# Performance work log

Hardware: AMD Instinct MI355X
Metric: run time of the kernel (lower is better)

The kernel has to match this reference:

```python
import jax, jax.numpy as jnp
import numpy as np

EPS = 1e-6


def _hungarian(cost):
    """Min-cost rectangular assignment (Kuhn-Munkres with potentials).
    Returns (row_ind, col_ind) matching min(n, m) pairs, like scipy's
    linear_sum_assignment. Cost matrices here are tiny (<= 7x7)."""
    cost = np.asarray(cost, dtype=np.float64)
    transposed = False
    if cost.shape[0] > cost.shape[1]:
        cost = cost.T
        transposed = True
    n, m = cost.shape
    INF = 1e18
    u = np.zeros(n + 1)
    v = np.zeros(m + 1)
    p = np.zeros(m + 1, dtype=np.int64)   # p[j] = row matched to col j (1-indexed)
    way = np.zeros(m + 1, dtype=np.int64)
    for i in range(1, n + 1):
        p[0] = i
        j0 = 0
        minv = np.full(m + 1, INF)
        used = np.zeros(m + 1, dtype=bool)
        while True:
            used[j0] = True
            i0 = p[j0]
            delta = INF
            j1 = 0
            for j in range(1, m + 1):
                if not used[j]:
                    cur = cost[i0 - 1, j - 1] - u[i0] - v[j]
                    if cur < minv[j]:
                        minv[j] = cur
                        way[j] = j0
                    if minv[j] < delta:
                        delta = minv[j]
                        j1 = j
            for j in range(m + 1):
                if used[j]:
                    u[p[j]] += delta
                    v[j] -= delta
                else:
                    minv[j] -= delta
            j0 = j1
            if p[j0] == 0:
                break
        while j0:
            j1 = way[j0]
            p[j0] = p[j1]
            j0 = j1
    rows, cols = [], []
    for j in range(1, m + 1):
        if p[j] != 0:
            rows.append(p[j] - 1)
            cols.append(j - 1)
    if transposed:
        rows, cols = cols, rows
    order = np.argsort(rows)
    return [rows[k] for k in order], [cols[k] for k in order]


def setup_inputs() -> dict:
    key = jax.random.key(0)
    kp, kg, kn = jax.random.split(key, 3)
    B, S, H, W = 32, 8, 256, 256
    pred_attn = jax.random.uniform(kp, (B, S, H, W), dtype=jnp.float32)  # soft slot attention
    gt_masks = jnp.round(jax.random.uniform(kg, (B, S, H, W), dtype=jnp.float32))  # binary GT
    num_objects = jax.random.randint(kn, (B,), 0, 8, dtype=jnp.int32)
    return {"pred_attn": pred_attn, "gt_masks": gt_masks, "num_objects": num_objects}


def _match(dice_mat, num_objects, num_gt):
    """Host-side Hungarian matching on the (negated) dice similarity matrix."""
    cost = -np.asarray(dice_mat)  # (B, P, G)
    nobj = np.asarray(num_objects)
    bi, pi, gi = [], [], []
    for b in range(cost.shape[0]):
        n = int(min(int(nobj[b]), num_gt))
        if n == 0:
            continue
        r, c = _hungarian(cost[b, :, :n])
        bi += [b] * len(r)
        pi += list(r)
        gi += list(c)
    return np.array(bi, np.int64), np.array(pi, np.int64), np.array(gi, np.int64)


def _losses(pred_attn, gt_masks, bi, pi, gi):
    B, S, H, W = pred_attn.shape
    # background dice loss (slot 0)
    bg_p = pred_attn[:, 0].reshape(B, -1)
    bg_g = gt_masks[:, 0].reshape(B, -1)
    inter = (bg_p * bg_g).sum(-1)
    union = bg_p.sum(-1) + bg_g.sum(-1)
    bg_loss = (1.0 - (2.0 * inter + EPS) / (union + EPS)).mean()
    # pairwise dice over all (pred_slot, gt_slot) fg pairs in one einsum
    fg_p = pred_attn[:, 1:].reshape(B, S - 1, -1)  # (B, P, HW)
    fg_g = gt_masks[:, 1:].reshape(B, S - 1, -1)   # (B, G, HW)
    inter_m = jnp.einsum('bpn,bgn->bpg', fg_p, fg_g)
    union_m = fg_p.sum(-1)[:, :, None] + fg_g.sum(-1)[:, None, :]
    dice_m = (2.0 * inter_m + EPS) / (union_m + EPS)  # (B, P, G)
    if bi.size:
        fg_loss = (1.0 - dice_m[bi, pi, gi]).mean()
    else:
        fg_loss = jnp.float32(0.0)
    return bg_loss, fg_loss, dice_m


def reference(pred_attn, gt_masks, num_objects):
    BG_WEIGHT, FG_WEIGHT = 1.0, 1.0
    B, S, H, W = pred_attn.shape
    # build dice similarity matrix once (vectorized; replaces the double loop)
    _, _, dice_m = _losses(pred_attn, gt_masks,
                           np.array([], np.int64), np.array([], np.int64), np.array([], np.int64))
    bi, pi, gi = _match(jax.lax.stop_gradient(dice_m), num_objects, S - 1)
    bg_loss, fg_loss, _ = _losses(pred_attn, gt_masks, bi, pi, gi)
    return BG_WEIGHT * bg_loss + FG_WEIGHT * fg_loss
```

## Files before the change

### kernel.cpp

```cpp
#include <hip/hip_runtime.h>
#include <stdint.h>

#define EPSF 1e-6f

__device__ __forceinline__ float wave_sum_to_lane63(float x) {
  x += __int_as_float(__builtin_amdgcn_update_dpp(0, __float_as_int(x), 0x111, 0xf, 0xf, true));
  x += __int_as_float(__builtin_amdgcn_update_dpp(0, __float_as_int(x), 0x112, 0xf, 0xf, true));
  x += __int_as_float(__builtin_amdgcn_update_dpp(0, __float_as_int(x), 0x114, 0xf, 0xf, true));
  x += __int_as_float(__builtin_amdgcn_update_dpp(0, __float_as_int(x), 0x118, 0xf, 0xf, true));
  x += __int_as_float(__builtin_amdgcn_update_dpp(0, __float_as_int(x), 0x142, 0xa, 0xf, false));
  x += __int_as_float(__builtin_amdgcn_update_dpp(0, __float_as_int(x), 0x143, 0xc, 0xf, false));
  return x;
}

__device__ __forceinline__ float sum4(float4 a) {
  return (a.x + a.y) + (a.z + a.w);
}
__device__ __forceinline__ float dot4(float4 a, float4 b) {
  return a.x * b.x + a.y * b.y + a.z * b.z + a.w * b.w;
}

#define RSZ 1024

__global__ __launch_bounds__(256) void msl_pack(const float* __restrict__ gt,
                                                uint32_t* __restrict__ bits,
                                                int nwords) {
  const int w = blockIdx.x * 256 + threadIdx.x;
  if (w >= nwords) return;
  const float4* src = (const float4*)(gt + (size_t)w * 32);
  uint32_t u = 0;
#pragma unroll
  for (int q = 0; q < 8; ++q) {
    float4 x = src[q];
    u |= (x.x > 0.5f ? 1u : 0u) << (q * 4 + 0);
    u |= (x.y > 0.5f ? 1u : 0u) << (q * 4 + 1);
    u |= (x.z > 0.5f ? 1u : 0u) << (q * 4 + 2);
    u |= (x.w > 0.5f ? 1u : 0u) << (q * 4 + 3);
  }
  bits[w] = u;
}

__global__ __launch_bounds__(256) void msl_accum(const float* __restrict__ pred,
                                                 const uint32_t* __restrict__ bits,
                                                 float* __restrict__ acc, int HW) {
  __shared__ float sm[8 * RSZ];
  const int bx   = blockIdx.x;
  const int b    = blockIdx.y;
  const int tid  = threadIdx.x;
  const int wave = tid >> 6;
  const int lane = tid & 63;

  const size_t base = (size_t)b * 8 * (size_t)HW;
  const float* Pr = pred + base + (size_t)bx * RSZ;
  const int wordsPerStream = HW >> 5;
  const int wbase = bx * (RSZ >> 5);

#pragma unroll
  for (int j = 0; j < 2; ++j) {
    const int s = wave * 2 + j;
    const float* sbase = Pr + (size_t)s * HW;
#pragma unroll
    for (int k = 0; k < 4; ++k) {
      const float* gp = sbase + k * 256 + lane * 4;
      float* lp = &sm[s * RSZ + k * 256];
      __builtin_amdgcn_global_load_lds(
          (const __attribute__((address_space(1))) void*)gp,
          (__attribute__((address_space(3))) void*)lp, 16, 0, 0);
    }
  }
  __builtin_amdgcn_s_waitcnt(0x0F70);
  __syncthreads();

  const int t4 = tid * 4;
  float4 pa[8];
#pragma unroll
  for (int p = 0; p < 8; ++p) pa[p] = *(const float4*)&sm[p * RSZ + t4];

  float sp[8], sg[8];
#pragma unroll
  for (int p = 0; p < 8; ++p) sp[p] = sum4(pa[p]);

  float a_bg = 0.0f;
  float af[7][7];
#pragma unroll
  for (int p = 0; p < 7; ++p)
#pragma unroll
    for (int g = 0; g < 7; ++g) af[p][g] = 0.0f;

#pragma unroll
  for (int g = 0; g < 8; ++g) {
    const uint32_t w = bits[(size_t)(b * 8 + g) * wordsPerStream + wbase + (tid >> 3)];
    const uint32_t nib = (w >> ((tid & 7) * 4)) & 0xFu;
    sg[g] = (float)__popc(nib);
    float4 m;
    m.x = (nib & 1u) ? 1.0f : 0.0f;
    m.y = (nib & 2u) ? 1.0f : 0.0f;
    m.z = (nib & 4u) ? 1.0f : 0.0f;
    m.w = (nib & 8u) ? 1.0f : 0.0f;
    if (g == 0) {
      a_bg = dot4(pa[0], m);
    } else {
#pragma unroll
      for (int p = 1; p < 8; ++p)
        af[p - 1][g - 1] += dot4(pa[p], m);
    }
  }

  float v[66];
  v[0] = a_bg;
#pragma unroll
  for (int p = 0; p < 7; ++p)
#pragma unroll
    for (int g = 0; g < 7; ++g) v[1 + p * 7 + g] = af[p][g];
#pragma unroll
  for (int s = 0; s < 8; ++s) { v[50 + s] = sp[s]; v[58 + s] = sg[s]; }

  __syncthreads();
  float* red = sm;
#pragma unroll
  for (int k = 0; k < 66; ++k) {
    float x = wave_sum_to_lane63(v[k]);
    if (lane == 63) red[wave * 66 + k] = x;
  }
  __syncthreads();

  if (tid < 66) {
    float s = red[0 * 66 + tid] + red[1 * 66 + tid] +
              red[2 * 66 + tid] + red[3 * 66 + tid];
    atomicAdd(&acc[b * 66 + tid], s);
  }
}

__global__ __launch_bounds__(1024) void msl_final(const float* __restrict__ acc,
                                                  const int* __restrict__ nobj,
                                                  float* __restrict__ out, int B) {
  __shared__ float a[32][68];
  __shared__ float dp[32][130];
  __shared__ float dice[32][52];
  __shared__ float r_bg[32];
  __shared__ float r_ds[32];
  __shared__ int   r_n[32];

  const int batch = threadIdx.x >> 5;
  const int lane  = threadIdx.x & 31;
  const bool act  = (batch < B);

  if (act) {
    for (int k = lane; k < 66; k += 32) a[batch][k] = acc[batch * 66 + k];
  }
  __syncthreads();

  if (act) {
    for (int k = lane; k < 49; k += 32) {
      int p = k / 7, g = k % 7;
      dice[batch][k] = (2.0f * a[batch][1 + k] + EPSF) /
                       (a[batch][51 + p] + a[batch][59 + g] + EPSF);
    }
    if (lane == 0) {
      float u = a[batch][50] + a[batch][58];
      r_bg[batch] = 1.0f - (2.0f * a[batch][0] + EPSF) / (u + EPSF);
      int n = nobj[batch];
      n = n < 0 ? 0 : (n > 7 ? 7 : n);
      r_n[batch] = n;
      r_ds[batch] = 0.0f;
      dp[batch][0] = 0.0f;
    }
  }
  __syncthreads();
  const int n = act ? r_n[batch] : 0;

  for (int c = 1; c <= 7; ++c) {
    if (act && c <= n) {
      for (int mask = lane; mask < 128; mask += 32) {
        if (__popc(mask) == c) {
          float best = -1e30f;
#pragma unroll
          for (int r = 0; r < 7; ++r) {
            if (mask & (1 << r)) {
              float cand = dp[batch][mask ^ (1 << r)] + dice[batch][r * 7 + (c - 1)];
              best = fmaxf(best, cand);
            }
          }
          dp[batch][mask] = best;
        }
      }
    }
    __syncthreads();
  }

  float best = -1e30f;
  if (act && n > 0) {
    for (int mask = lane; mask < 128; mask += 32)
      if (__popc(mask) == n) best = fmaxf(best, dp[batch][mask]);
  }
#pragma unroll
  for (int off = 16; off > 0; off >>= 1)
    best = fmaxf(best, __shfl_down(best, off, 32));
  if (act && lane == 0 && n > 0) r_ds[batch] = best;
  __syncthreads();

  if (threadIdx.x == 0) {
    float bg = 0.0f, ds = 0.0f;
    int cnt = 0;
    for (int b = 0; b < B; ++b) { bg += r_bg[b]; ds += r_ds[b]; cnt += r_n[b]; }
    float fg = cnt > 0 ? ((float)cnt - ds) / (float)cnt : 0.0f;
    out[0] = bg / (float)B + fg;
  }
}

extern "C" void kernel_launch(void* const* d_in, const int* in_sizes, int n_in,
                              void* d_out, int out_size, void* d_ws, size_t ws_size,
                              hipStream_t stream) {
  const float* pred = (const float*)d_in[0];
  const float* gt   = (const float*)d_in[1];
  const int*   nobj = (const int*)d_in[2];
  float* out = (float*)d_out;

  const int B  = in_sizes[2];
  const int HW = in_sizes[0] / (B * 8);

  float*    acc  = (float*)d_ws;
  uint32_t* bits = (uint32_t*)d_ws + 4096;

  const int nwords = (B * 8 * HW) >> 5;
  msl_pack<<<dim3((nwords + 255) / 256), dim3(256), 0, stream>>>(gt, bits, nwords);

  const int GRIDX = HW / RSZ;
  msl_accum<<<dim3(GRIDX, B), dim3(256), 0, stream>>>(pred, bits, acc, HW);

  msl_final<<<dim3(1), dim3(32 * B), 0, stream>>>(acc, nobj, out, B);
}
```

Measured before the change: 167.5 us.

## Split accumulation per pred slot and move GT popcount sums into pack kernel

```diff
diff --git a/kernel.cpp b/kernel.cpp
--- a/kernel.cpp
+++ b/kernel.cpp
@@ -20,13 +20,10 @@
   return a.x * b.x + a.y * b.y + a.z * b.z + a.w * b.w;
 }
 
-#define RSZ 1024
-
 __global__ __launch_bounds__(256) void msl_pack(const float* __restrict__ gt,
                                                 uint32_t* __restrict__ bits,
-                                                int nwords) {
+                                                float* __restrict__ acc) {
   const int w = blockIdx.x * 256 + threadIdx.x;
-  if (w >= nwords) return;
   const float4* src = (const float4*)(gt + (size_t)w * 32);
   uint32_t u = 0;
 #pragma unroll
@@ -38,96 +35,67 @@
     u |= (x.w > 0.5f ? 1u : 0u) << (q * 4 + 3);
   }
   bits[w] = u;
+
+  float pc = wave_sum_to_lane63((float)__popc(u));
+  if ((threadIdx.x & 63) == 63) {
+    const int stream = w >> 11;
+    const int b = stream >> 3, g = stream & 7;
+    atomicAdd(&acc[b * 66 + 58 + g], pc);
+  }
 }
 
 __global__ __launch_bounds__(256) void msl_accum(const float* __restrict__ pred,
                                                  const uint32_t* __restrict__ bits,
                                                  float* __restrict__ acc, int HW) {
-  __shared__ float sm[8 * RSZ];
-  const int bx   = blockIdx.x;
-  const int b    = blockIdx.y;
   const int tid  = threadIdx.x;
   const int wave = tid >> 6;
   const int lane = tid & 63;
 
-  const size_t base = (size_t)b * 8 * (size_t)HW;
-  const float* Pr = pred + base + (size_t)bx * RSZ;
-  const int wordsPerStream = HW >> 5;
-  const int wbase = bx * (RSZ >> 5);
-
-#pragma unroll
-  for (int j = 0; j < 2; ++j) {
-    const int s = wave * 2 + j;
-    const float* sbase = Pr + (size_t)s * HW;
-#pragma unroll
-    for (int k = 0; k < 4; ++k) {
-      const float* gp = sbase + k * 256 + lane * 4;
-      float* lp = &sm[s * RSZ + k * 256];
-      __builtin_amdgcn_global_load_lds(
-          (const __attribute__((address_space(1))) void*)gp,
-          (__attribute__((address_space(3))) void*)lp, 16, 0, 0);
-    }
-  }
-  __builtin_amdgcn_s_waitcnt(0x0F70);
-  __syncthreads();
-
-  const int t4 = tid * 4;
-  float4 pa[8];
-#pragma unroll
-  for (int p = 0; p < 8; ++p) pa[p] = *(const float4*)&sm[p * RSZ + t4];
-
-  float sp[8], sg[8];
-#pragma unroll
-  for (int p = 0; p < 8; ++p) sp[p] = sum4(pa[p]);
-
-  float a_bg = 0.0f;
-  float af[7][7];
-#pragma unroll
-  for (int p = 0; p < 7; ++p)
-#pragma unroll
-    for (int g = 0; g < 7; ++g) af[p][g] = 0.0f;
-
+  const int cps   = HW >> 10;
+  const int chunk = blockIdx.x % cps;
+  const int ps    = blockIdx.x / cps;
+  const int p     = ps & 7;
+  const int b     = ps >> 3;
+
+  const int pos4 = chunk * 256 + tid;
+  const float4 pa = ((const float4*)(pred + (size_t)ps * HW))[pos4];
+
+  const int widx = pos4 >> 3;
+  const int nsh  = (pos4 & 7) * 4;
+  const uint32_t* bstream = bits + (size_t)(b * 8) * (HW >> 5);
+  const int wps = HW >> 5;
+
+  float v[9];
+  v[8] = sum4(pa);
 #pragma unroll
   for (int g = 0; g < 8; ++g) {
-    const uint32_t w = bits[(size_t)(b * 8 + g) * wordsPerStream + wbase + (tid >> 3)];
-    const uint32_t nib = (w >> ((tid & 7) * 4)) & 0xFu;
-    sg[g] = (float)__popc(nib);
+    const uint32_t word = bstream[(size_t)g * wps + widx];
+    const uint32_t nib = (word >> nsh) & 0xFu;
     float4 m;
     m.x = (nib & 1u) ? 1.0f : 0.0f;
     m.y = (nib & 2u) ? 1.0f : 0.0f;
     m.z = (nib & 4u) ? 1.0f : 0.0f;
     m.w = (nib & 8u) ? 1.0f : 0.0f;
-    if (g == 0) {
-      a_bg = dot4(pa[0], m);
-    } else {
-#pragma unroll
-      for (int p = 1; p < 8; ++p)
-        af[p - 1][g - 1] += dot4(pa[p], m);
-    }
-  }
-
-  float v[66];
-  v[0] = a_bg;
-#pragma unroll
-  for (int p = 0; p < 7; ++p)
-#pragma unroll
-    for (int g = 0; g < 7; ++g) v[1 + p * 7 + g] = af[p][g];
-#pragma unroll
-  for (int s = 0; s < 8; ++s) { v[50 + s] = sp[s]; v[58 + s] = sg[s]; }
-
-  __syncthreads();
-  float* red = sm;
-#pragma unroll
-  for (int k = 0; k < 66; ++k) {
+    v[g] = dot4(pa, m);
+  }
+
+  __shared__ float red[4][9];
+#pragma unroll
+  for (int k = 0; k < 9; ++k) {
     float x = wave_sum_to_lane63(v[k]);
-    if (lane == 63) red[wave * 66 + k] = x;
-  }
-  __syncthreads();
-
-  if (tid < 66) {
-    float s = red[0 * 66 + tid] + red[1 * 66 + tid] +
-              red[2 * 66 + tid] + red[3 * 66 + tid];
-    atomicAdd(&acc[b * 66 + tid], s);
+    if (lane == 63) red[wave][k] = x;
+  }
+  __syncthreads();
+
+  if (tid < 9) {
+    float s = red[0][tid] + red[1][tid] + red[2][tid] + red[3][tid];
+    if (tid == 8) {
+      atomicAdd(&acc[b * 66 + 50 + p], s);
+    } else if (p == 0) {
+      if (tid == 0) atomicAdd(&acc[b * 66 + 0], s);
+    } else if (tid >= 1) {
+      atomicAdd(&acc[b * 66 + 1 + (p - 1) * 7 + (tid - 1)], s);
+    }
   }
 }
 
@@ -223,10 +191,10 @@
   uint32_t* bits = (uint32_t*)d_ws + 4096;
 
   const int nwords = (B * 8 * HW) >> 5;
-  msl_pack<<<dim3((nwords + 255) / 256), dim3(256), 0, stream>>>(gt, bits, nwords);
-
-  const int GRIDX = HW / RSZ;
-  msl_accum<<<dim3(GRIDX, B), dim3(256), 0, stream>>>(pred, bits, acc, HW);
+  msl_pack<<<dim3(nwords / 256), dim3(256), 0, stream>>>(gt, bits, acc);
+
+  const int nblocks = (B * 8 * HW) >> 10;
+  msl_accum<<<dim3(nblocks), dim3(256), 0, stream>>>(pred, bits, acc, HW);
 
   msl_final<<<dim3(1), dim3(32 * B), 0, stream>>>(acc, nobj, out, B);
 }
```

New measurement: 173.6 us. 1.04x slower.
